# Kernel tuning notes

Hardware: AMD Instinct MI355X
Metric: run time of the kernel (lower is better)

The kernel has to match this reference:

```python
import jax, jax.numpy as jnp
import numpy as np

B, T, D, NH, FF, L, NCLS, CELL = 4, 64, 128, 4, 512, 2, 7, 64
DIMS = (600, 342, 300)


def layernorm(x, g, b, eps=1e-5):
    m = jnp.mean(x, -1, keepdims=True)
    v = jnp.mean((x - m) ** 2, -1, keepdims=True)
    return (x - m) / jnp.sqrt(v + eps) * g + b


def mha(x, Wqkv, bqkv, Wo, bo):
    N, S, Dm = x.shape
    hd = Dm // NH
    q, k, v = jnp.split(x @ Wqkv + bqkv, 3, axis=-1)
    q = q.reshape(N, S, NH, hd).transpose(0, 2, 1, 3) / jnp.float32(hd) ** 0.5
    k = k.reshape(N, S, NH, hd).transpose(0, 2, 1, 3)
    v = v.reshape(N, S, NH, hd).transpose(0, 2, 1, 3)
    att = jax.nn.softmax(jnp.einsum('nhqd,nhkd->nhqk', q, k), axis=-1)
    o = jnp.einsum('nhqk,nhkd->nhqd', att, v).transpose(0, 2, 1, 3).reshape(N, S, Dm)
    return o @ Wo + bo


def _l2norm(x):
    return x / jnp.maximum(jnp.linalg.norm(x, axis=-1, keepdims=True), 1e-12)


def _model(x_text, x_vis, x_aud, Wp_text, bp_text, Wp_vis, bp_vis, Wp_aud, bp_aud,
           lang1, lang2, Wl1, bl1, Wl2, bl2, phase_text, phase_vis, phase_aud,
           t_Wqkv, t_bqkv, t_Wo, t_bo, t_g1, t_b1, t_W1, t_bf1, t_W2, t_bf2, t_g2, t_b2,
           meas_r, meas_i, fc_W1, fc_b1, fc_W2, fc_b2):
    b, t = x_text.shape[0], x_text.shape[1]
    # modality projections + ReLU
    reps = [jax.nn.relu(x @ W + bb) for x, W, bb in
            ((x_text, Wp_text, bp_text), (x_vis, Wp_vis, bp_vis), (x_aud, Wp_aud, bp_aud))]
    l1 = jnp.broadcast_to(lang1, (b, t, lang1.shape[-1]))
    l2 = jnp.broadcast_to(lang2, (b, t, lang2.shape[-1]))
    lrep1 = jax.nn.relu(l1 @ Wl1 + bl1)
    lrep2 = jax.nn.relu(l2 @ Wl2 + bl2)
    amps = [_l2norm(r) for r in reps]
    lamp1, lamp2 = _l2norm(lrep1), _l2norm(lrep2)
    # phase embedding: smask is all-ones so index is always 0 -> single learned phase vector
    phases = [jnp.broadcast_to(p, (b, t, D)) for p in (phase_text, phase_vis, phase_aud)]
    cmul = lambda ph, a: (a * jnp.cos(ph), a * jnp.sin(ph))
    pure = [cmul(ph, a) for ph, a in zip(phases, amps)]
    ls1 = cmul(phases[0], lamp1)
    ls2 = cmul(phases[0], lamp2)
    # Hadamard gate analog on (real, imag)
    s2 = jnp.float32(2.0) ** -0.5
    h1 = ((ls1[0] + ls1[1]) * s2, (ls1[0] - ls1[1]) * s2)
    h2 = ((ls2[0] + ls2[1]) * s2, (ls2[0] - ls2[1]) * s2)
    # CNOT-style entanglement: complex elementwise product, renormalized to a pure state
    er = h1[0] * h2[0] - h1[1] * h2[1]
    ei = h1[0] * h2[1] + h1[1] * h2[0]
    en = jnp.maximum(jnp.sqrt(jnp.sum(er * er + ei * ei, -1, keepdims=True)), 1e-12)
    ent = (er / en, ei / en)

    def outer(st):  # rho = v v^dagger, v = r + i*im
        r, i = st
        rr = jnp.einsum('btd,bte->btde', r, r) + jnp.einsum('btd,bte->btde', i, i)
        ri = jnp.einsum('btd,bte->btde', i, r) - jnp.einsum('btd,bte->btde', r, i)
        return rr, ri

    mats = [outer(s) for s in pure] + [outer(ent)]
    w = jnp.concatenate([jnp.linalg.norm(r, axis=-1, keepdims=True)
                         for r in reps + [lrep1]], -1)
    w = jax.nn.softmax(w, -1)  # [B,T,4]
    rho_r = sum(w[..., m:m + 1, None] * mats[m][0] for m in range(4))
    rho_i = sum(w[..., m:m + 1, None] * mats[m][1] for m in range(4))
    # seq blocks: same block applied independently per timestep to real and imag parts
    # -> vectorize the Python loop over T (and the real/imag pair) into one batch dim
    x = jnp.concatenate([rho_r, rho_i], 0).reshape(2 * b * t, D, D)
    for l in range(L):
        x = layernorm(x + mha(x, t_Wqkv[l], t_bqkv[l], t_Wo[l], t_bo[l]), t_g1[l], t_b1[l])
        x = layernorm(x + (jax.nn.relu(x @ t_W1[l] + t_bf1[l]) @ t_W2[l] + t_bf2[l]),
                      t_g2[l], t_b2[l])
    x = x.reshape(2, b, t, D, D)
    rho_r, rho_i = x[0], x[1]
    # quantum measurement: p_k = Re(v_k^dagger rho v_k), v_k normalized complex vectors
    mn = jnp.maximum(jnp.sqrt(jnp.sum(meas_r ** 2 + meas_i ** 2, -1, keepdims=True)), 1e-12)
    vr, vi = meas_r / mn, meas_i / mn  # [K=D, D]
    ar = jnp.einsum('btde,ke->btkd', rho_r, vr) - jnp.einsum('btde,ke->btkd', rho_i, vi)
    ai = jnp.einsum('btde,ke->btkd', rho_r, vi) + jnp.einsum('btde,ke->btkd', rho_i, vr)
    probs = jnp.einsum('kd,btkd->btk', vr, ar) + jnp.einsum('kd,btkd->btk', vi, ai)
    logits = jax.nn.relu(probs @ fc_W1 + fc_b1) @ fc_W2 + fc_b2
    return jax.nn.log_softmax(logits, -1)  # [B,T,NCLS]


def setup_inputs():
    key = jax.random.key(0)
    ks = iter(jax.random.split(key, 32))
    rn = lambda shape, s=0.05: jax.random.normal(next(ks), shape, dtype=jnp.float32) * s
    z = lambda shape: jnp.zeros(shape, jnp.float32)
    o = lambda shape: jnp.ones(shape, jnp.float32)
    return dict(
        x_text=rn((B, T, DIMS[0]), 1.0), x_vis=rn((B, T, DIMS[1]), 1.0), x_aud=rn((B, T, DIMS[2]), 1.0),
        Wp_text=rn((DIMS[0], D)), bp_text=z((D,)),
        Wp_vis=rn((DIMS[1], D)), bp_vis=z((D,)),
        Wp_aud=rn((DIMS[2], D)), bp_aud=z((D,)),
        lang1=rn((1, 1, DIMS[2]), 1.0), lang2=rn((1, 1, DIMS[2]), 1.0),
        Wl1=rn((DIMS[2], D)), bl1=z((D,)), Wl2=rn((DIMS[2], D)), bl2=z((D,)),
        phase_text=rn((D,), 1.0), phase_vis=rn((D,), 1.0), phase_aud=rn((D,), 1.0),
        t_Wqkv=rn((L, D, 3 * D)), t_bqkv=z((L, 3 * D)),
        t_Wo=rn((L, D, D)), t_bo=z((L, D)),
        t_g1=o((L, D)), t_b1=z((L, D)),
        t_W1=rn((L, D, FF)), t_bf1=z((L, FF)),
        t_W2=rn((L, FF, D)), t_bf2=z((L, D)),
        t_g2=o((L, D)), t_b2=z((L, D)),
        meas_r=rn((D, D), 1.0), meas_i=rn((D, D), 1.0),
        fc_W1=rn((D, CELL)), fc_b1=z((CELL,)), fc_W2=rn((CELL, NCLS)), fc_b2=z((NCLS,)),
    )


def reference(x_text, x_vis, x_aud, Wp_text, bp_text, Wp_vis, bp_vis, Wp_aud, bp_aud,
              lang1, lang2, Wl1, bl1, Wl2, bl2, phase_text, phase_vis, phase_aud,
              t_Wqkv, t_bqkv, t_Wo, t_bo, t_g1, t_b1, t_W1, t_bf1, t_W2, t_bf2, t_g2, t_b2,
              meas_r, meas_i, fc_W1, fc_b1, fc_W2, fc_b2):
    return _model(x_text, x_vis, x_aud, Wp_text, bp_text, Wp_vis, bp_vis, Wp_aud, bp_aud,
                  lang1, lang2, Wl1, bl1, Wl2, bl2, phase_text, phase_vis, phase_aud,
                  t_Wqkv, t_bqkv, t_Wo, t_bo, t_g1, t_b1, t_W1, t_bf1, t_W2, t_bf2, t_g2, t_b2,
                  meas_r, meas_i, fc_W1, fc_b1, fc_W2, fc_b2)
```

## Files before the change

kernel.cpp:

```cpp
#include <hip/hip_runtime.h>
#include <hip/hip_bf16.h>

typedef __hip_bfloat16 bf16;
typedef short short8 __attribute__((ext_vector_type(8)));
typedef float f32x4 __attribute__((ext_vector_type(4)));

__device__ __forceinline__ float b2f(bf16 v){ return __bfloat162float(v); }

__device__ __forceinline__ short f2bs(float f){
  union { __hip_bfloat16 b; short s; } u; u.b = __float2bfloat16(f); return u.s;
}
__device__ __forceinline__ float bs2f(short s){
  union { short s; __hip_bfloat16 b; } u; u.s = s; return __bfloat162float(u.b);
}

__device__ __forceinline__ float wred_sum(float v){
  #pragma unroll
  for (int o = 32; o > 0; o >>= 1) v += __shfl_xor(v, o, 64);
  return v;
}

__device__ __forceinline__ void gload_lds16(const void* g, void* l){
  __builtin_amdgcn_global_load_lds((const __attribute__((address_space(1))) unsigned*)g,
                                   (__attribute__((address_space(3))) unsigned*)l, 16, 0, 0);
}

__device__ __forceinline__ unsigned swzA(unsigned a){ return a ^ (((a >> 8) & 7u) << 4); }
__device__ __forceinline__ unsigned swzB(unsigned a){ return a ^ (((a >> 7) & 3u) << 4); }

template<int DIMN>
__device__ void modality(const float* x, const float* W, const float* bia, const float* ph,
                         float* PURE, float* RNORM, int m, int bt, float* xs, float* red)
{
  int tid = threadIdx.x;
  for (int i = tid; i < DIMN; i += 128) xs[i] = x[bt*DIMN + i];
  __syncthreads();
  float a0 = 0.f, a1 = 0.f, a2 = 0.f, a3 = 0.f;
  int k = 0;
  for (; k + 4 <= DIMN; k += 4){
    a0 = fmaf(xs[k],   W[(k  )*128 + tid], a0);
    a1 = fmaf(xs[k+1], W[(k+1)*128 + tid], a1);
    a2 = fmaf(xs[k+2], W[(k+2)*128 + tid], a2);
    a3 = fmaf(xs[k+3], W[(k+3)*128 + tid], a3);
  }
  for (; k < DIMN; k++) a0 = fmaf(xs[k], W[k*128 + tid], a0);
  float acc = bia[tid] + ((a0 + a1) + (a2 + a3));
  float rep = fmaxf(acc, 0.f);
  float s = wred_sum(rep*rep);
  int wid = tid >> 6, lane = tid & 63;
  if (lane == 0) red[wid] = s;
  __syncthreads();
  float nrm = sqrtf(red[0] + red[1]);
  float amp = rep / fmaxf(nrm, 1e-12f);
  float p = ph[tid];
  PURE[bt*768 + m*128 + tid]       = amp * cosf(p);
  PURE[bt*768 + (3+m)*128 + tid]   = amp * sinf(p);
  if (tid == 0) RNORM[bt*4 + m] = nrm;
}

__global__ void prep_kernel(
    const float* __restrict__ Wqkv, const float* __restrict__ Wo,
    const float* __restrict__ W1, const float* __restrict__ W2,
    short* __restrict__ WqkvT, short* __restrict__ WoT,
    short* __restrict__ W1T, short* __restrict__ W2T,
    const float* xt, const float* xv, const float* xa,
    const float* Wpt, const float* bpt, const float* Wpv, const float* bpv,
    const float* Wpa, const float* bpa,
    const float* pht, const float* phv, const float* pha,
    float* PURE, float* RNORM,
    const float* l1, const float* l2,
    const float* Wl1, const float* bl1, const float* Wl2, const float* bl2,
    float* LANGB,
    const float* mr, const float* mi, float* VMEAS, short* VMEASB)
{
  __shared__ float xs[600];
  __shared__ float xs2a[300];
  __shared__ float red[4];
  __shared__ float tile[32][33];
  int b = blockIdx.x, tid = threadIdx.x;

  if (b < 384){
    int l = b / 192, bb = b - l*192;
    const float* in; short* out; int K, N, kt, nt_;
    bool isW2 = false;
    if (bb < 48)      { in = Wqkv; out = WqkvT; K = 128; N = 384; kt = bb & 3;  nt_ = bb >> 2; }
    else if (bb < 64) { int t = bb-48;  in = Wo; out = WoT; K = 128; N = 128; kt = t & 3;  nt_ = t >> 2; }
    else if (bb < 128){ int t = bb-64;  in = W1; out = W1T; K = 128; N = 512; kt = t & 3;  nt_ = t >> 2; }
    else              { int t = bb-128; in = W2; out = W2T; K = 512; N = 128; kt = t & 15; nt_ = t >> 4; isW2 = true; }
    int base = l * K * N;
    int kk0 = kt*32, nn0 = nt_*32;
    int r0 = tid >> 5, c = tid & 31;
    #pragma unroll
    for (int i = 0; i < 8; i++){
      int r = i*4 + r0;
      tile[r][c] = in[base + (kk0 + r)*N + nn0 + c];
    }
    __syncthreads();
    #pragma unroll
    for (int i = 0; i < 8; i++){
      int rr = i*4 + r0;
      float v = tile[c][rr];
      int oi;
      if (!isW2) oi = (nn0 + rr)*K + kk0 + c;
      else       oi = kt*4096 + (nn0 + rr)*32 + c;
      out[base + oi] = f2bs(v);
    }
    return;
  }
  if (b < 1152){
    int idx = b - 384;
    int bt = idx & 255, m = idx >> 8;
    if (m == 0)      modality<600>(xt, Wpt, bpt, pht, PURE, RNORM, 0, bt, xs, red);
    else if (m == 1) modality<342>(xv, Wpv, bpv, phv, PURE, RNORM, 1, bt, xs, red);
    else             modality<300>(xa, Wpa, bpa, pha, PURE, RNORM, 2, bt, xs, red);
    return;
  }
  if (b >= 1153){
    int k = b - 1153;
    float a = mr[k*128 + tid], bb2 = mi[k*128 + tid];
    float ws = wred_sum(a*a + bb2*bb2);
    int wid = tid >> 6, lane = tid & 63;
    if (lane == 0) red[wid] = ws;
    __syncthreads();
    float inv = 1.f / fmaxf(sqrtf(red[0] + red[1]), 1e-12f);
    float vr = a * inv, vi = bb2 * inv;
    int i = k*128 + tid;
    VMEAS[i]          = vr;
    VMEAS[16384 + i]  = vi;
    VMEASB[i]         = f2bs(vr);
    VMEASB[16384 + i] = f2bs(vi);
    VMEASB[32768 + i] = f2bs(-vi);
    return;
  }
  for (int i = tid; i < 300; i += 128){ xs[i] = l1[i]; xs2a[i] = l2[i]; }
  __syncthreads();
  float p10=0,p11=0,p12=0,p13=0, p20=0,p21=0,p22=0,p23=0;
  for (int k = 0; k < 300; k += 4){
    p10 = fmaf(xs[k],    Wl1[(k  )*128+tid], p10);
    p11 = fmaf(xs[k+1],  Wl1[(k+1)*128+tid], p11);
    p12 = fmaf(xs[k+2],  Wl1[(k+2)*128+tid], p12);
    p13 = fmaf(xs[k+3],  Wl1[(k+3)*128+tid], p13);
    p20 = fmaf(xs2a[k],  Wl2[(k  )*128+tid], p20);
    p21 = fmaf(xs2a[k+1],Wl2[(k+1)*128+tid], p21);
    p22 = fmaf(xs2a[k+2],Wl2[(k+2)*128+tid], p22);
    p23 = fmaf(xs2a[k+3],Wl2[(k+3)*128+tid], p23);
  }
  float a1 = bl1[tid] + ((p10+p11)+(p12+p13));
  float a2 = bl2[tid] + ((p20+p21)+(p22+p23));
  a1 = fmaxf(a1, 0.f); a2 = fmaxf(a2, 0.f);
  int wid = tid >> 6, lane = tid & 63;
  float s1 = wred_sum(a1*a1), s2 = wred_sum(a2*a2);
  if (lane == 0){ red[wid] = s1; red[2+wid] = s2; }
  __syncthreads();
  float n1 = sqrtf(red[0] + red[1]);
  float n2 = sqrtf(red[2] + red[3]);
  float lamp1 = a1 / fmaxf(n1, 1e-12f);
  float lamp2 = a2 / fmaxf(n2, 1e-12f);
  float ph = pht[tid];
  float c = cosf(ph), s = sinf(ph);
  const float s2c = 0.70710678118654752f;
  float h1r = (lamp1*c + lamp1*s)*s2c, h1i = (lamp1*c - lamp1*s)*s2c;
  float h2r = (lamp2*c + lamp2*s)*s2c, h2i = (lamp2*c - lamp2*s)*s2c;
  float er = h1r*h2r - h1i*h2i;
  float ei = h1r*h2i + h1i*h2r;
  __syncthreads();
  float se = wred_sum(er*er + ei*ei);
  if (lane == 0) red[wid] = se;
  __syncthreads();
  float en = fmaxf(sqrtf(red[0] + red[1]), 1e-12f);
  LANGB[tid]       = er / en;
  LANGB[128 + tid] = ei / en;
  if (tid == 0) LANGB[256] = n1;
}

__global__ __launch_bounds__(256) void rho_kernel(const float* PURE, const float* RNORM,
                                                  const float* LANGB, short* Xb)
{
  __shared__ float rv[4][128], iv[4][128], wsm[4];
  int bt = blockIdx.x >> 1, half = blockIdx.x & 1;
  int tid = threadIdx.x;
  for (int i = tid; i < 1024; i += 256){
    int d = i & 127;
    if (i < 768){ int m = i >> 7; float v = PURE[bt*768 + i];
                  if (m < 3) rv[m][d] = v; else iv[m-3][d] = v; }
    else if (i < 896) rv[3][d] = LANGB[d];
    else              iv[3][d] = LANGB[128 + d];
  }
  if (tid == 0){
    float n0 = RNORM[bt*4+0], n1 = RNORM[bt*4+1], n2 = RNORM[bt*4+2], n3 = LANGB[256];
    float mx = fmaxf(fmaxf(n0, n1), fmaxf(n2, n3));
    float e0 = __expf(n0-mx), e1 = __expf(n1-mx), e2 = __expf(n2-mx), e3 = __expf(n3-mx);
    float inv = 1.f / (e0+e1+e2+e3);
    wsm[0]=e0*inv; wsm[1]=e1*inv; wsm[2]=e2*inv; wsm[3]=e3*inv;
  }
  __syncthreads();
  float w0 = wsm[0], w1 = wsm[1], w2 = wsm[2], w3 = wsm[3];
  int lo = half*8192, hi = lo + 8192;
  for (int idx = lo + tid; idx < hi; idx += 256){
    int d = idx >> 7, e = idx & 127;
    float rr = 0.f, ri = 0.f;
    {
      float rd=rv[0][d], re=rv[0][e], id=iv[0][d], ie=iv[0][e];
      rr = fmaf(w0, rd*re + id*ie, rr); ri = fmaf(w0, id*re - rd*ie, ri);
    }{
      float rd=rv[1][d], re=rv[1][e], id=iv[1][d], ie=iv[1][e];
      rr = fmaf(w1, rd*re + id*ie, rr); ri = fmaf(w1, id*re - rd*ie, ri);
    }{
      float rd=rv[2][d], re=rv[2][e], id=iv[2][d], ie=iv[2][e];
      rr = fmaf(w2, rd*re + id*ie, rr); ri = fmaf(w2, id*re - rd*ie, ri);
    }{
      float rd=rv[3][d], re=rv[3][e], id=iv[3][d], ie=iv[3][e];
      rr = fmaf(w3, rd*re + id*ie, rr); ri = fmaf(w3, id*re - rd*ie, ri);
    }
    Xb[(size_t)bt*16384 + idx]        = f2bs(rr);
    Xb[(size_t)(256+bt)*16384 + idx]  = f2bs(ri);
  }
}

__global__ __launch_bounds__(256) void attn_kernel(const short* __restrict__ Xb,
    const short* __restrict__ WqkvT, const float* __restrict__ bqkv,
    bf16* __restrict__ ATTO)
{
  __shared__ __align__(16) char lds_raw[43520];
  short* Vt = (short*)(lds_raw);
  short* Qs = (short*)(lds_raw + 8704);
  short* Ks = (short*)(lds_raw + 18944);
  short* Ps = (short*)(lds_raw + 8704);

  const int n = blockIdx.x, h = blockIdx.y;
  const int tid = threadIdx.x;
  const int wid = tid >> 6, lane = tid & 63;
  const int l15 = lane & 15, quad = lane >> 4;
  const int wb = __builtin_amdgcn_readfirstlane(wid);
  const short* xn = Xb + (size_t)n*16384;
  const char* Wbase = (const char*)WqkvT;

  short8 afr[2][4];
  #pragma unroll
  for (int mi = 0; mi < 2; mi++)
    #pragma unroll
    for (int ks = 0; ks < 4; ks++){
      int row = (wid*2 + mi)*16 + l15;
      afr[mi][ks] = *(const short8*)(xn + row*128 + ks*32 + quad*8);
    }
  #pragma unroll
  for (int j = 0; j < 6; j++){
    int seg = wb*6 + j;
    int slab = seg >> 3;
    unsigned off = (unsigned)((seg & 7)*1024);
    unsigned gbase = (unsigned)((slab*128 + h*32)*256);
    gload_lds16(Wbase + gbase + swzA(off + (unsigned)(lane*16)),
                lds_raw + seg*1024);
  }
  __syncthreads();

  f32x4 acc[2][6];
  #pragma unroll
  for (int mi = 0; mi < 2; mi++)
    #pragma unroll
    for (int nt = 0; nt < 6; nt++){
      f32x4 z = {0.f, 0.f, 0.f, 0.f}; acc[mi][nt] = z;
    }

  #pragma unroll
  for (int ks = 0; ks < 4; ks++){
    #pragma unroll
    for (int nt = 0; nt < 6; nt++){
      int slab = nt >> 1;
      int col = (nt & 1)*16 + l15;
      unsigned a = (unsigned)(col*256 + ks*64 + quad*16);
      short8 bfr = *(const short8*)(lds_raw + slab*8192 + swzA(a));
      #pragma unroll
      for (int mi = 0; mi < 2; mi++)
        acc[mi][nt] = __builtin_amdgcn_mfma_f32_16x16x32_bf16(afr[mi][ks], bfr, acc[mi][nt], 0, 0, 0);
    }
  }
  __syncthreads();

  #pragma unroll
  for (int nt = 0; nt < 6; nt++){
    int sec = nt >> 1;
    int cl = (nt & 1)*16 + l15;
    float bias = bqkv[sec*128 + h*32 + cl];
    #pragma unroll
    for (int mi = 0; mi < 2; mi++){
      int rowb = (wid*2 + mi)*16 + quad*4;
      #pragma unroll
      for (int r = 0; r < 4; r++){
        float v = acc[mi][nt][r] + bias;
        int row = rowb + r;
        if (sec == 0)      Qs[row*40 + cl] = f2bs(v * 0.17677669529663687f);
        else if (sec == 1) Ks[row*40 + cl] = f2bs(v);
        else               Vt[cl*136 + row] = f2bs(v);
      }
    }
  }
  __syncthreads();

  f32x4 s[2][8];
  {
    short8 qf[2];
    #pragma unroll
    for (int mi = 0; mi < 2; mi++){
      int row = (wid*2 + mi)*16 + l15;
      qf[mi] = *(const short8*)(Qs + row*40 + quad*8);
    }
    #pragma unroll
    for (int nt = 0; nt < 8; nt++){
      int kr = nt*16 + l15;
      short8 kf = *(const short8*)(Ks + kr*40 + quad*8);
      #pragma unroll
      for (int mi = 0; mi < 2; mi++){
        f32x4 z = {0.f, 0.f, 0.f, 0.f};
        s[mi][nt] = __builtin_amdgcn_mfma_f32_16x16x32_bf16(qf[mi], kf, z, 0, 0, 0);
      }
    }
  }

  #pragma unroll
  for (int mi = 0; mi < 2; mi++){
    #pragma unroll
    for (int r = 0; r < 4; r++){
      float m = -1e30f;
      #pragma unroll
      for (int nt = 0; nt < 8; nt++) m = fmaxf(m, s[mi][nt][r]);
      #pragma unroll
      for (int o = 1; o < 16; o <<= 1) m = fmaxf(m, __shfl_xor(m, o, 64));
      float sum = 0.f;
      #pragma unroll
      for (int nt = 0; nt < 8; nt++){
        float p = __expf(s[mi][nt][r] - m);
        s[mi][nt][r] = p; sum += p;
      }
      #pragma unroll
      for (int o = 1; o < 16; o <<= 1) sum += __shfl_xor(sum, o, 64);
      float inv = 1.f / sum;
      #pragma unroll
      for (int nt = 0; nt < 8; nt++) s[mi][nt][r] *= inv;
    }
  }
  __syncthreads();

  #pragma unroll
  for (int mi = 0; mi < 2; mi++){
    int rowb = (wid*2 + mi)*16 + quad*4;
    #pragma unroll
    for (int nt = 0; nt < 8; nt++){
      int col = nt*16 + l15;
      #pragma unroll
      for (int r = 0; r < 4; r++)
        Ps[(rowb + r)*136 + col] = f2bs(s[mi][nt][r]);
    }
  }
  __syncthreads();

  f32x4 o_[2][2];
  #pragma unroll
  for (int mi = 0; mi < 2; mi++)
    #pragma unroll
    for (int n2 = 0; n2 < 2; n2++){
      f32x4 z = {0.f, 0.f, 0.f, 0.f}; o_[mi][n2] = z;
    }
  #pragma unroll
  for (int ks = 0; ks < 4; ks++){
    short8 pf[2];
    #pragma unroll
    for (int mi = 0; mi < 2; mi++){
      int row = (wid*2 + mi)*16 + l15;
      pf[mi] = *(const short8*)(Ps + row*136 + ks*32 + quad*8);
    }
    #pragma unroll
    for (int n2 = 0; n2 < 2; n2++){
      short8 vf = *(const short8*)(Vt + (n2*16 + l15)*136 + ks*32 + quad*8);
      #pragma unroll
      for (int mi = 0; mi < 2; mi++)
        o_[mi][n2] = __builtin_amdgcn_mfma_f32_16x16x32_bf16(pf[mi], vf, o_[mi][n2], 0, 0, 0);
    }
  }
  bf16* on = ATTO + (size_t)n*16384;
  #pragma unroll
  for (int mi = 0; mi < 2; mi++){
    int rowb = (wid*2 + mi)*16 + quad*4;
    #pragma unroll
    for (int n2 = 0; n2 < 2; n2++){
      int col = h*32 + n2*16 + l15;
      #pragma unroll
      for (int r = 0; r < 4; r++)
        on[(rowb + r)*128 + col] = __float2bfloat16(o_[mi][n2][r]);
    }
  }
}

__global__ __launch_bounds__(256, 2) void proj_ffn_kernel(const bf16* __restrict__ SRC,
    short* __restrict__ Xb, const short* __restrict__ WoT,
    const float* __restrict__ bo, const float* __restrict__ g1v,
    const float* __restrict__ bb1,
    const short* __restrict__ W1T, const float* __restrict__ bf1,
    const short* __restrict__ W2C, const float* __restrict__ bf2,
    const float* __restrict__ g2v, const float* __restrict__ bb2)
{
  __shared__ __align__(16) char lds_raw[65536];
  __shared__ float bf1L[512];
  const int n = blockIdx.x, tid = threadIdx.x;
  const int wid = tid >> 6, lane = tid & 63;
  const int l15 = lane & 15, quad = lane >> 4;
  const int wb = __builtin_amdgcn_readfirstlane(wid);
  const short* an = (const short*)SRC + (size_t)n*16384;
  short* xn = Xb + (size_t)n*16384;
  char* XsB = lds_raw + 32768;
  short* Hs = (short*)(lds_raw + 32768);

  short8 af[2][4];
  #pragma unroll
  for (int mi = 0; mi < 2; mi++)
    #pragma unroll
    for (int ks = 0; ks < 4; ks++){
      int row = wid*32 + mi*16 + l15;
      af[mi][ks] = *(const short8*)(an + row*128 + ks*32 + quad*8);
    }
  #pragma unroll
  for (int j = 0; j < 8; j++){
    unsigned L = (unsigned)(j*4096 + wb*1024 + lane*16);
    gload_lds16((const char*)WoT + swzA(L), lds_raw + (j*4096 + wb*1024));
    gload_lds16((const char*)xn  + swzA(L), XsB + (j*4096 + wb*1024));
  }
  for (int i = tid; i < 512; i += 256) bf1L[i] = bf1[i];
  float bov[8], g1a[8], b1a[8];
  #pragma unroll
  for (int nt = 0; nt < 8; nt++){
    int col = nt*16 + l15;
    bov[nt] = bo[col]; g1a[nt] = g1v[col]; b1a[nt] = bb1[col];
  }
  __syncthreads();

  f32x4 Y[2][8];
  #pragma unroll
  for (int mi = 0; mi < 2; mi++)
    #pragma unroll
    for (int nt = 0; nt < 8; nt++){ f32x4 z = {0.f,0.f,0.f,0.f}; Y[mi][nt] = z; }
  #pragma unroll
  for (int ks = 0; ks < 4; ks++){
    #pragma unroll
    for (int nt = 0; nt < 8; nt++){
      unsigned a = (unsigned)((nt*16 + l15)*256 + ks*64 + quad*16);
      short8 bh = *(const short8*)(lds_raw + swzA(a));
      #pragma unroll
      for (int mi = 0; mi < 2; mi++)
        Y[mi][nt] = __builtin_amdgcn_mfma_f32_16x16x32_bf16(af[mi][ks], bh, Y[mi][nt], 0, 0, 0);
    }
  }
  __syncthreads();

  #pragma unroll
  for (int j = 0; j < 2; j++){
    unsigned L = (unsigned)(j*4096 + wb*1024 + lane*16);
    gload_lds16((const char*)W1T + swzA(L), lds_raw + (j*4096 + wb*1024));
    gload_lds16((const char*)W2C + swzB(L), lds_raw + (8192 + j*4096 + wb*1024));
  }

  unsigned yv1p[2][4][4];
  #pragma unroll
  for (int mi = 0; mi < 2; mi++){
    #pragma unroll
    for (int r = 0; r < 4; r++){
      int row = wid*32 + mi*16 + quad*4 + r;
      float yv[8]; float S = 0.f, Q = 0.f;
      #pragma unroll
      for (int nt = 0; nt < 8; nt++){
        int col = nt*16 + l15;
        float res = bs2f(*(const short*)(XsB + swzA((unsigned)(row*256 + col*2))));
        float y = Y[mi][nt][r] + bov[nt] + res;
        yv[nt] = y; S += y; Q += y*y;
      }
      #pragma unroll
      for (int o = 1; o < 16; o <<= 1){ S += __shfl_xor(S, o, 64); Q += __shfl_xor(Q, o, 64); }
      float m = S * (1.f/128.f);
      float var = Q * (1.f/128.f) - m*m;
      float inv = rsqrtf(var + 1e-5f);
      #pragma unroll
      for (int nt = 0; nt < 8; nt++){
        int col = nt*16 + l15;
        short ob = f2bs((yv[nt] - m) * inv * g1a[nt] + b1a[nt]);
        *(short*)(XsB + swzA((unsigned)(row*256 + col*2))) = ob;
        unsigned u = (unsigned)(unsigned short)ob;
        if ((nt & 1) == 0) yv1p[mi][r][nt>>1] = u;
        else               yv1p[mi][r][nt>>1] |= (u << 16);
      }
    }
  }

  short8 af2[2][4];
  #pragma unroll
  for (int mi = 0; mi < 2; mi++)
    #pragma unroll
    for (int ks = 0; ks < 4; ks++){
      int row = wid*32 + mi*16 + l15;
      unsigned a = (unsigned)(row*256 + ks*64 + quad*16);
      af2[mi][ks] = *(const short8*)(XsB + swzA(a));
    }
  __syncthreads();

  f32x4 Y2[2][8];
  #pragma unroll
  for (int mi = 0; mi < 2; mi++)
    #pragma unroll
    for (int nt = 0; nt < 8; nt++){ f32x4 z = {0.f,0.f,0.f,0.f}; Y2[mi][nt] = z; }

  for (int c = 0; c < 16; c++){
    const int cb = c & 1;
    if (c < 15){
      const int nb = cb ^ 1;
      #pragma unroll
      for (int j = 0; j < 2; j++){
        unsigned L = (unsigned)(j*4096 + wb*1024 + lane*16);
        gload_lds16((const char*)W1T + (unsigned)((c+1)*8192) + swzA(L),
                    lds_raw + (nb*16384 + j*4096 + wb*1024));
        gload_lds16((const char*)W2C + (unsigned)((c+1)*8192) + swzB(L),
                    lds_raw + (nb*16384 + 8192 + j*4096 + wb*1024));
      }
      asm volatile("s_waitcnt vmcnt(4)" ::: "memory");
    } else {
      asm volatile("s_waitcnt vmcnt(0)" ::: "memory");
    }
    __builtin_amdgcn_sched_barrier(0);
    __builtin_amdgcn_s_barrier();
    __builtin_amdgcn_sched_barrier(0);

    const char* bW1 = lds_raw + cb*16384;
    const char* bW2 = lds_raw + cb*16384 + 8192;

    f32x4 Hc[2][2];
    #pragma unroll
    for (int mi = 0; mi < 2; mi++)
      #pragma unroll
      for (int nt2 = 0; nt2 < 2; nt2++){ f32x4 z = {0.f,0.f,0.f,0.f}; Hc[mi][nt2] = z; }
    #pragma unroll
    for (int ks = 0; ks < 4; ks++){
      #pragma unroll
      for (int nt2 = 0; nt2 < 2; nt2++){
        unsigned a = (unsigned)((nt2*16 + l15)*256 + ks*64 + quad*16);
        short8 bh = *(const short8*)(bW1 + swzA(a));
        #pragma unroll
        for (int mi = 0; mi < 2; mi++)
          Hc[mi][nt2] = __builtin_amdgcn_mfma_f32_16x16x32_bf16(af2[mi][ks], bh, Hc[mi][nt2], 0, 0, 0);
      }
    }
    float b1v0 = bf1L[c*32 + l15];
    float b1v1 = bf1L[c*32 + 16 + l15];
    #pragma unroll
    for (int nt2 = 0; nt2 < 2; nt2++){
      int col = nt2*16 + l15;
      float b1v = nt2 ? b1v1 : b1v0;
      #pragma unroll
      for (int mi = 0; mi < 2; mi++){
        int rowb = wid*32 + mi*16 + quad*4;
        #pragma unroll
        for (int r = 0; r < 4; r++)
          Hs[(rowb + r)*40 + col] = f2bs(fmaxf(Hc[mi][nt2][r] + b1v, 0.f));
      }
    }
    short8 ph[2];
    #pragma unroll
    for (int mi = 0; mi < 2; mi++){
      int row = wid*32 + mi*16 + l15;
      ph[mi] = *(const short8*)(Hs + row*40 + quad*8);
    }
    #pragma unroll
    for (int nt = 0; nt < 8; nt++){
      unsigned a = (unsigned)((nt*16 + l15)*64 + quad*16);
      short8 bh = *(const short8*)(bW2 + swzB(a));
      #pragma unroll
      for (int mi = 0; mi < 2; mi++)
        Y2[mi][nt] = __builtin_amdgcn_mfma_f32_16x16x32_bf16(ph[mi], bh, Y2[mi][nt], 0, 0, 0);
    }
    __builtin_amdgcn_sched_barrier(0);
    __builtin_amdgcn_s_barrier();
    __builtin_amdgcn_sched_barrier(0);
  }

  {
    float b2v[8], gv[8], bbv[8];
    #pragma unroll
    for (int nt = 0; nt < 8; nt++){
      int col = nt*16 + l15;
      b2v[nt] = bf2[col]; gv[nt] = g2v[col]; bbv[nt] = bb2[col];
    }
    #pragma unroll
    for (int mi = 0; mi < 2; mi++){
      #pragma unroll
      for (int r = 0; r < 4; r++){
        int row = wid*32 + mi*16 + quad*4 + r;
        float yv[8]; float S = 0.f, Q = 0.f;
        #pragma unroll
        for (int nt = 0; nt < 8; nt++){
          unsigned u = yv1p[mi][r][nt>>1];
          short rs = (short)((nt & 1) ? (u >> 16) : (u & 0xffffu));
          float y = Y2[mi][nt][r] + b2v[nt] + bs2f(rs);
          yv[nt] = y; S += y; Q += y*y;
        }
        #pragma unroll
        for (int o = 1; o < 16; o <<= 1){ S += __shfl_xor(S, o, 64); Q += __shfl_xor(Q, o, 64); }
        float m = S * (1.f/128.f);
        float var = Q * (1.f/128.f) - m*m;
        float inv = rsqrtf(var + 1e-5f);
        #pragma unroll
        for (int nt = 0; nt < 8; nt++){
          int col = nt*16 + l15;
          xn[row*128 + col] = f2bs((yv[nt] - m) * inv * gv[nt] + bbv[nt]);
        }
      }
    }
  }
}

__global__ __launch_bounds__(256) void probs_head_kernel(const short* __restrict__ Xb,
    const float* __restrict__ VMEAS, const short* __restrict__ VMEASB,
    const float* __restrict__ W1, const float* __restrict__ b1,
    const float* __restrict__ W2, const float* __restrict__ b2,
    float* __restrict__ out)
{
  __shared__ __align__(16) char lds_raw[24576];
  __shared__ float sp[128];
  __shared__ float hsh[64];
  __shared__ float lg[7];
  __shared__ float mred[2];
  const int bt = blockIdx.x, tid = threadIdx.x;
  const int wid = tid >> 6, lane = tid & 63;
  const int l15 = lane & 15, quad = lane >> 4;
  const int wb = __builtin_amdgcn_readfirstlane(wid);
  const short* R = Xb + (size_t)bt*16384;
  const short* I = Xb + (size_t)(256+bt)*16384;

  if (tid < 128) sp[tid] = 0.f;

  short8 aR[2][4], aI[2][4];
  #pragma unroll
  for (int z = 0; z < 2; z++){
    int drow = z*64 + wid*16 + l15;
    #pragma unroll
    for (int ks = 0; ks < 4; ks++){
      aR[z][ks] = *(const short8*)(R + drow*128 + ks*32 + quad*8);
      aI[z][ks] = *(const short8*)(I + drow*128 + ks*32 + quad*8);
    }
  }

  #define STAGE_NT(nt_, buf_)                                                  \
    { _Pragma("unroll")                                                        \
      for (int j = 0; j < 3; j++){                                             \
        int seg = wb*3 + j;                                         \
        int s = seg >> 2;                                       \
        unsigned off = (unsigned)((seg & 3)*1024);                             \
        gload_lds16((const char*)VMEASB + s*32768 + (nt_)*4096 +               \
                      swzA(off + (unsigned)(lane*16)),                         \
                    lds_raw + (buf_)*12288 + s*4096 + (int)off);               \
      } }

  STAGE_NT(0, 0)
  __syncthreads();

  const int db0 = wid*16 + quad*4;

  for (int nt = 0; nt < 8; nt++){
    const int cb = nt & 1;
    int k = nt*16 + l15;
    f32x4 vR0 = *(const f32x4*)(VMEAS + k*128 + db0);
    f32x4 vI0 = *(const f32x4*)(VMEAS + 16384 + k*128 + db0);
    f32x4 vR1 = *(const f32x4*)(VMEAS + k*128 + 64 + db0);
    f32x4 vI1 = *(const f32x4*)(VMEAS + 16384 + k*128 + 64 + db0);
    if (nt < 7){
      STAGE_NT(nt+1, cb^1)
      asm volatile("s_waitcnt vmcnt(3)" ::: "memory");
    } else {
      asm volatile("s_waitcnt vmcnt(0)" ::: "memory");
    }
    __builtin_amdgcn_sched_barrier(0);
    __builtin_amdgcn_s_barrier();
    __builtin_amdgcn_sched_barrier(0);

    const char* bvr = lds_raw + cb*12288;
    const char* bvi = bvr + 4096;
    const char* bnv = bvr + 8192;

    f32x4 Ar0 = {0.f,0.f,0.f,0.f}, Ai0 = {0.f,0.f,0.f,0.f};
    f32x4 Ar1 = {0.f,0.f,0.f,0.f}, Ai1 = {0.f,0.f,0.f,0.f};
    #pragma unroll
    for (int ks = 0; ks < 4; ks++){
      unsigned a = swzA((unsigned)(l15*256 + ks*64 + quad*16));
      short8 b_vr = *(const short8*)(bvr + a);
      short8 b_vi = *(const short8*)(bvi + a);
      short8 b_nv = *(const short8*)(bnv + a);
      Ar0 = __builtin_amdgcn_mfma_f32_16x16x32_bf16(aR[0][ks], b_vr, Ar0, 0, 0, 0);
      Ar0 = __builtin_amdgcn_mfma_f32_16x16x32_bf16(aI[0][ks], b_nv, Ar0, 0, 0, 0);
      Ai0 = __builtin_amdgcn_mfma_f32_16x16x32_bf16(aR[0][ks], b_vi, Ai0, 0, 0, 0);
      Ai0 = __builtin_amdgcn_mfma_f32_16x16x32_bf16(aI[0][ks], b_vr, Ai0, 0, 0, 0);
      Ar1 = __builtin_amdgcn_mfma_f32_16x16x32_bf16(aR[1][ks], b_vr, Ar1, 0, 0, 0);
      Ar1 = __builtin_amdgcn_mfma_f32_16x16x32_bf16(aI[1][ks], b_nv, Ar1, 0, 0, 0);
      Ai1 = __builtin_amdgcn_mfma_f32_16x16x32_bf16(aR[1][ks], b_vi, Ai1, 0, 0, 0);
      Ai1 = __builtin_amdgcn_mfma_f32_16x16x32_bf16(aI[1][ks], b_vr, Ai1, 0, 0, 0);
    }

    float pv = 0.f;
    #pragma unroll
    for (int r = 0; r < 4; r++){
      pv += vR0[r]*Ar0[r] + vI0[r]*Ai0[r];
      pv += vR1[r]*Ar1[r] + vI1[r]*Ai1[r];
    }
    pv += __shfl_xor(pv, 16, 64);
    pv += __shfl_xor(pv, 32, 64);
    if (quad == 0) atomicAdd(&sp[nt*16 + l15], pv);

    __builtin_amdgcn_sched_barrier(0);
    __builtin_amdgcn_s_barrier();
    __builtin_amdgcn_sched_barrier(0);
  }
  #undef STAGE_NT

  __syncthreads();
  if (tid < 64){
    float a0 = b1[tid], a1 = 0.f, a2 = 0.f, a3 = 0.f;
    for (int d = 0; d < 128; d += 4){
      a0 = fmaf(sp[d  ], W1[(d  )*64 + tid], a0);
      a1 = fmaf(sp[d+1], W1[(d+1)*64 + tid], a1);
      a2 = fmaf(sp[d+2], W1[(d+2)*64 + tid], a2);
      a3 = fmaf(sp[d+3], W1[(d+3)*64 + tid], a3);
    }
    hsh[tid] = fmaxf((a0 + a1) + (a2 + a3), 0.f);
  }
  __syncthreads();
  if (tid < 7){
    float a = b2[tid];
    for (int j = 0; j < 64; j++) a = fmaf(hsh[j], W2[j*7 + tid], a);
    lg[tid] = a;
  }
  __syncthreads();
  if (tid == 0){
    float M = -1e30f;
    for (int c = 0; c < 7; c++) M = fmaxf(M, lg[c]);
    float S = 0.f;
    for (int c = 0; c < 7; c++) S += __expf(lg[c] - M);
    mred[0] = M; mred[1] = logf(S);
  }
  __syncthreads();
  if (tid < 7) out[bt*7 + tid] = lg[tid] - mred[0] - mred[1];
}

extern "C" void kernel_launch(void* const* d_in, const int* in_sizes, int n_in,
                              void* d_out, int out_size, void* d_ws, size_t ws_size,
                              hipStream_t stream)
{
  (void)in_sizes; (void)n_in; (void)out_size; (void)ws_size;
  const float* xt   = (const float*)d_in[0];
  const float* xv   = (const float*)d_in[1];
  const float* xa   = (const float*)d_in[2];
  const float* Wpt  = (const float*)d_in[3];
  const float* bpt  = (const float*)d_in[4];
  const float* Wpv  = (const float*)d_in[5];
  const float* bpv  = (const float*)d_in[6];
  const float* Wpa  = (const float*)d_in[7];
  const float* bpa  = (const float*)d_in[8];
  const float* l1   = (const float*)d_in[9];
  const float* l2   = (const float*)d_in[10];
  const float* Wl1  = (const float*)d_in[11];
  const float* bl1  = (const float*)d_in[12];
  const float* Wl2  = (const float*)d_in[13];
  const float* bl2  = (const float*)d_in[14];
  const float* pht  = (const float*)d_in[15];
  const float* phv  = (const float*)d_in[16];
  const float* pha  = (const float*)d_in[17];
  const float* Wqkv = (const float*)d_in[18];
  const float* bqkv = (const float*)d_in[19];
  const float* Wo   = (const float*)d_in[20];
  const float* bo   = (const float*)d_in[21];
  const float* g1   = (const float*)d_in[22];
  const float* b1   = (const float*)d_in[23];
  const float* W1   = (const float*)d_in[24];
  const float* bf1  = (const float*)d_in[25];
  const float* W2   = (const float*)d_in[26];
  const float* bf2  = (const float*)d_in[27];
  const float* g2   = (const float*)d_in[28];
  const float* b2   = (const float*)d_in[29];
  const float* mr   = (const float*)d_in[30];
  const float* mi   = (const float*)d_in[31];
  const float* fcW1 = (const float*)d_in[32];
  const float* fcb1 = (const float*)d_in[33];
  const float* fcW2 = (const float*)d_in[34];
  const float* fcb2 = (const float*)d_in[35];
  float* out = (float*)d_out;

  char* wsb = (char*)d_ws;
  short* Xb     = (short*)(wsb);
  bf16*  ATTO   = (bf16*) (wsb + 16777216);
  float* PURE   = (float*)(wsb + 33554432);
  float* RNORM  = (float*)(wsb + 34340864);
  float* LANGB  = (float*)(wsb + 34344960);
  float* VMEAS  = (float*)(wsb + 34347008);
  short* WqkvT  = (short*)(wsb + 34740224);
  short* WoT    = (short*)(wsb + 34936832);
  short* W1T    = (short*)(wsb + 35002368);
  short* W2T    = (short*)(wsb + 35264512);
  short* VMEASB = (short*)(wsb + 35526656);

  prep_kernel<<<1281, 128, 0, stream>>>(Wqkv, Wo, W1, W2, WqkvT, WoT, W1T, W2T,
                                        xt, xv, xa, Wpt, bpt, Wpv, bpv, Wpa, bpa,
                                        pht, phv, pha, PURE, RNORM,
                                        l1, l2, Wl1, bl1, Wl2, bl2, LANGB,
                                        mr, mi, VMEAS, VMEASB);

  rho_kernel<<<512, 256, 0, stream>>>(PURE, RNORM, LANGB, Xb);

  for (int l = 0; l < 2; l++){
    attn_kernel<<<dim3(512, 4), 256, 0, stream>>>(Xb, WqkvT + (size_t)l*49152,
                                                  bqkv + (size_t)l*384, ATTO);
    proj_ffn_kernel<<<512, 256, 0, stream>>>(ATTO, Xb,
                                             WoT + (size_t)l*16384,
                                             bo + (size_t)l*128, g1 + (size_t)l*128,
                                             b1 + (size_t)l*128,
                                             W1T + (size_t)l*65536, bf1 + (size_t)l*512,
                                             W2T + (size_t)l*65536, bf2 + (size_t)l*128,
                                             g2 + (size_t)l*128, b2 + (size_t)l*128);
  }

  probs_head_kernel<<<256, 256, 0, stream>>>(Xb, VMEAS, VMEASB,
                                             fcW1, fcb1, fcW2, fcb2, out);
}
```

Baseline: 289.8 us.

## Swizzle attention LDS, raise occupancy hint, and simplify pipeline barriers

```diff
diff --git a/kernel.cpp b/kernel.cpp
--- a/kernel.cpp
+++ b/kernel.cpp
@@ -217,15 +217,15 @@
   }
 }
 
-__global__ __launch_bounds__(256) void attn_kernel(const short* __restrict__ Xb,
+__global__ __launch_bounds__(256, 4) void attn_kernel(const short* __restrict__ Xb,
     const short* __restrict__ WqkvT, const float* __restrict__ bqkv,
     bf16* __restrict__ ATTO)
 {
-  __shared__ __align__(16) char lds_raw[43520];
-  short* Vt = (short*)(lds_raw);
-  short* Qs = (short*)(lds_raw + 8704);
-  short* Ks = (short*)(lds_raw + 18944);
-  short* Ps = (short*)(lds_raw + 8704);
+  __shared__ __align__(16) char lds_raw[40960];
+  char*  VtB = lds_raw;
+  short* Qs  = (short*)(lds_raw + 8192);
+  short* Ks  = (short*)(lds_raw + 18432);
+  char*  PsB = lds_raw + 8192;
 
   const int n = blockIdx.x, h = blockIdx.y;
   const int tid = threadIdx.x;
@@ -291,7 +291,7 @@
         int row = rowb + r;
         if (sec == 0)      Qs[row*40 + cl] = f2bs(v * 0.17677669529663687f);
         else if (sec == 1) Ks[row*40 + cl] = f2bs(v);
-        else               Vt[cl*136 + row] = f2bs(v);
+        else               *(short*)(VtB + swzA((unsigned)(cl*256 + row*2))) = f2bs(v);
       }
     }
   }
@@ -349,7 +349,7 @@
       int col = nt*16 + l15;
       #pragma unroll
       for (int r = 0; r < 4; r++)
-        Ps[(rowb + r)*136 + col] = f2bs(s[mi][nt][r]);
+        *(short*)(PsB + swzA((unsigned)((rowb + r)*256 + col*2))) = f2bs(s[mi][nt][r]);
     }
   }
   __syncthreads();
@@ -367,11 +367,11 @@
     #pragma unroll
     for (int mi = 0; mi < 2; mi++){
       int row = (wid*2 + mi)*16 + l15;
-      pf[mi] = *(const short8*)(Ps + row*136 + ks*32 + quad*8);
+      pf[mi] = *(const short8*)(PsB + swzA((unsigned)(row*256 + ks*64 + quad*16)));
     }
     #pragma unroll
     for (int n2 = 0; n2 < 2; n2++){
-      short8 vf = *(const short8*)(Vt + (n2*16 + l15)*136 + ks*32 + quad*8);
+      short8 vf = *(const short8*)(VtB + swzA((unsigned)((n2*16 + l15)*256 + ks*64 + quad*16)));
       #pragma unroll
       for (int mi = 0; mi < 2; mi++)
         o_[mi][n2] = __builtin_amdgcn_mfma_f32_16x16x32_bf16(pf[mi], vf, o_[mi][n2], 0, 0, 0);
@@ -400,7 +400,6 @@
     const float* __restrict__ g2v, const float* __restrict__ bb2)
 {
   __shared__ __align__(16) char lds_raw[65536];
-  __shared__ float bf1L[512];
   const int n = blockIdx.x, tid = threadIdx.x;
   const int wid = tid >> 6, lane = tid & 63;
   const int l15 = lane & 15, quad = lane >> 4;
@@ -424,7 +423,6 @@
     gload_lds16((const char*)WoT + swzA(L), lds_raw + (j*4096 + wb*1024));
     gload_lds16((const char*)xn  + swzA(L), XsB + (j*4096 + wb*1024));
   }
-  for (int i = tid; i < 512; i += 256) bf1L[i] = bf1[i];
   float bov[8], g1a[8], b1a[8];
   #pragma unroll
   for (int nt = 0; nt < 8; nt++){
@@ -518,14 +516,7 @@
         gload_lds16((const char*)W2C + (unsigned)((c+1)*8192) + swzB(L),
                     lds_raw + (nb*16384 + 8192 + j*4096 + wb*1024));
       }
-      asm volatile("s_waitcnt vmcnt(4)" ::: "memory");
-    } else {
-      asm volatile("s_waitcnt vmcnt(0)" ::: "memory");
-    }
-    __builtin_amdgcn_sched_barrier(0);
-    __builtin_amdgcn_s_barrier();
-    __builtin_amdgcn_sched_barrier(0);
-
+    }
     const char* bW1 = lds_raw + cb*16384;
     const char* bW2 = lds_raw + cb*16384 + 8192;
 
@@ -545,8 +536,8 @@
           Hc[mi][nt2] = __builtin_amdgcn_mfma_f32_16x16x32_bf16(af2[mi][ks], bh, Hc[mi][nt2], 0, 0, 0);
       }
     }
-    float b1v0 = bf1L[c*32 + l15];
-    float b1v1 = bf1L[c*32 + 16 + l15];
+    float b1v0 = bf1[c*32 + l15];
+    float b1v1 = bf1[c*32 + 16 + l15];
     #pragma unroll
     for (int nt2 = 0; nt2 < 2; nt2++){
       int col = nt2*16 + l15;
@@ -573,9 +564,7 @@
       for (int mi = 0; mi < 2; mi++)
         Y2[mi][nt] = __builtin_amdgcn_mfma_f32_16x16x32_bf16(ph[mi], bh, Y2[mi][nt], 0, 0, 0);
     }
-    __builtin_amdgcn_sched_barrier(0);
-    __builtin_amdgcn_s_barrier();
-    __builtin_amdgcn_sched_barrier(0);
+    if (c < 15) __syncthreads();
   }
 
   {
@@ -667,15 +656,7 @@
     f32x4 vI0 = *(const f32x4*)(VMEAS + 16384 + k*128 + db0);
     f32x4 vR1 = *(const f32x4*)(VMEAS + k*128 + 64 + db0);
     f32x4 vI1 = *(const f32x4*)(VMEAS + 16384 + k*128 + 64 + db0);
-    if (nt < 7){
-      STAGE_NT(nt+1, cb^1)
-      asm volatile("s_waitcnt vmcnt(3)" ::: "memory");
-    } else {
-      asm volatile("s_waitcnt vmcnt(0)" ::: "memory");
-    }
-    __builtin_amdgcn_sched_barrier(0);
-    __builtin_amdgcn_s_barrier();
-    __builtin_amdgcn_sched_barrier(0);
+    if (nt < 7) STAGE_NT(nt+1, cb^1)
 
     const char* bvr = lds_raw + cb*12288;
     const char* bvi = bvr + 4096;
@@ -709,13 +690,10 @@
     pv += __shfl_xor(pv, 32, 64);
     if (quad == 0) atomicAdd(&sp[nt*16 + l15], pv);
 
-    __builtin_amdgcn_sched_barrier(0);
-    __builtin_amdgcn_s_barrier();
-    __builtin_amdgcn_sched_barrier(0);
+    __syncthreads();
   }
   #undef STAGE_NT
 
-  __syncthreads();
   if (tid < 64){
     float a0 = b1[tid], a1 = 0.f, a2 = 0.f, a3 = 0.f;
     for (int d = 0; d < 128; d += 4){
```

Measured after the change: 294.3 us. Within noise of the previous version (+1.6%).
